# Optimization experiments

Hardware: AMD Instinct MI355X
Metric: run time of the kernel (lower is better)

## Reference

```python
import jax, jax.numpy as jnp
import numpy as np

B, T, E, H = 2, 2048, 1024, 16
D = E // H
K_KEEP = 391
RECENCY = 64
SCALE = D ** -0.5


def setup_inputs() -> dict:
    key = jax.random.key(0)
    k1, k2, k3 = jax.random.split(key, 3)
    x = jax.random.normal(k1, (B, T, E), jnp.float32)
    W_attn = jax.random.normal(k2, (3 * E, E), jnp.float32) * 0.02  # torch Linear weight [out,in]
    W_proj = jax.random.normal(k3, (E, E), jnp.float32) * 0.02
    return {"x": x, "W_attn": W_attn, "W_proj": W_proj}


def reference(x, W_attn, W_proj):
    b, t, c = x.shape
    qkv = x @ W_attn.T                      # [B,T,3E]
    q, k, v = jnp.split(qkv, 3, axis=-1)
    to_heads = lambda u: u.reshape(b, t, H, D).transpose(0, 2, 1, 3)  # [B,H,T,D]
    q, k, v = to_heads(q), to_heads(k), to_heads(v)

    # first pass: causal attention weights for importance scoring
    scores = jnp.einsum('bhqd,bhkd->bhqk', q, k) * SCALE
    causal = jnp.tril(jnp.ones((t, t), dtype=bool))
    scores = jnp.where(causal, scores, -jnp.inf)
    attn_w = jax.nn.softmax(scores, axis=-1)

    # mean importance over query dim, force-keep recent tokens
    imp = attn_w.mean(axis=2)               # [B,H,T]
    imp = imp.at[:, :, -RECENCY:].set(1.0)

    # top-k token selection per (batch, head)
    _, idx = jax.lax.top_k(imp, K_KEEP)     # [B,H,K]

    # gather pruned K/V
    K_keep = jnp.take_along_axis(k, idx[..., None], axis=2)  # [B,H,K,D]
    V_keep = jnp.take_along_axis(v, idx[..., None], axis=2)

    # second attention pass over pruned keys (no causal mask, matches legacy code)
    s2 = jnp.einsum('bhqd,bhkd->bhqk', q, K_keep) * SCALE
    a2 = jax.nn.softmax(s2, axis=-1)
    out = jnp.einsum('bhqk,bhkd->bhqd', a2, V_keep)          # [B,H,T,D]

    out = out.transpose(0, 2, 1, 3).reshape(b, t, c)
    return out @ W_proj.T
```

## Files before the change

kernel.cpp:

```cpp
#include <hip/hip_runtime.h>
#include <hip/hip_bf16.h>


#define TT 2048
#define EE 1024
#define HH 16
#define DD 64
#define KKEEP 391
#define REC 64
#define NBH 32
#define QSCALE 0.125f
#define KPAD 448

typedef short bf16x8 __attribute__((ext_vector_type(8)));
typedef _Float16 f16x8 __attribute__((ext_vector_type(8)));
typedef float f32x4 __attribute__((ext_vector_type(4)));

#define WAIT_VM(N) asm volatile("s_waitcnt vmcnt(" #N ")" ::: "memory")
#define WAIT_LGKM0 asm volatile("s_waitcnt lgkmcnt(0)" ::: "memory")
#define BAR() __builtin_amdgcn_s_barrier()

static __device__ inline unsigned short bf_rn(float x) {
  unsigned u = __float_as_uint(x);
  unsigned r = u + 0x7fffu + ((u >> 16) & 1u);
  return (unsigned short)(r >> 16);
}
static __device__ inline float bf_up(unsigned short h) {
  return __uint_as_float((unsigned)h << 16);
}
static __device__ inline unsigned pkf16(float a, float b) {
  union { _Float16 h[2]; unsigned u; } t;
  t.h[0] = (_Float16)a; t.h[1] = (_Float16)b; return t.u;
}
static __device__ inline void glds16(const void* g, void* l) {
  __builtin_amdgcn_global_load_lds(
      (const __attribute__((address_space(1))) void*)g,
      (__attribute__((address_space(3))) void*)l, 16, 0, 0);
}

static __device__ inline void split4(const float* __restrict__ src,
                                     unsigned short* __restrict__ ho,
                                     unsigned short* __restrict__ lo_, int i)
{
  float4 v = *reinterpret_cast<const float4*>(&src[i]);
  ushort4 hh, ll;
  float f;
  hh.x = bf_rn(v.x); f = bf_up(hh.x); ll.x = bf_rn(v.x - f);
  hh.y = bf_rn(v.y); f = bf_up(hh.y); ll.y = bf_rn(v.y - f);
  hh.z = bf_rn(v.z); f = bf_up(hh.z); ll.z = bf_rn(v.z - f);
  hh.w = bf_rn(v.w); f = bf_up(hh.w); ll.w = bf_rn(v.w - f);
  *reinterpret_cast<ushort4*>(&ho[i]) = hh;
  *reinterpret_cast<ushort4*>(&lo_[i]) = ll;
}

__global__ __launch_bounds__(256) void split_kernel(
    const float* __restrict__ src, unsigned short* __restrict__ ho,
    unsigned short* __restrict__ lo_, int n)
{
  int i = (blockIdx.x * 256 + threadIdx.x) * 4;
  const int stride = gridDim.x * 1024;
  for (; i < n; i += stride) split4(src, ho, lo_, i);
}

__global__ __launch_bounds__(256) void split2_kernel(
    const float* __restrict__ x, const float* __restrict__ wa,
    unsigned short* __restrict__ xh, unsigned short* __restrict__ xl,
    unsigned short* __restrict__ wh, unsigned short* __restrict__ wl)
{
  const int n1 = 4096 * 1024, n2 = 3072 * 1024;
  int i = (blockIdx.x * 256 + threadIdx.x) * 4;
  const int stride = gridDim.x * 1024;
  for (; i < n1 + n2; i += stride) {
    if (i < n1) split4(x, xh, xl, i);
    else        split4(wa, wh, wl, i - n1);
  }
}

template<bool VB, int MODE>
__global__ __launch_bounds__(256) void gemm_pipe(
    const unsigned short* __restrict__ Ah, const unsigned short* __restrict__ Al,
    const unsigned short* __restrict__ Bh, const unsigned short* __restrict__ Bl,
    float* __restrict__ Cc, unsigned short* __restrict__ Qho, unsigned short* __restrict__ Qlo,
    unsigned short* __restrict__ Kho, unsigned short* __restrict__ Klo,
    float* __restrict__ Vo, int M, int N, int Kd, int nOff)
{
  __shared__ __align__(16) unsigned short Ahs[2][128 * 32];
  __shared__ __align__(16) unsigned short Bhs[2][128 * 32];
  __shared__ __align__(16) unsigned short Als[VB ? 1 : 2][128 * 32];
  __shared__ __align__(16) unsigned short Bls[VB ? 1 : 2][128 * 32];
  const int tid = threadIdx.x;
  const int m0 = blockIdx.y * 128, n0 = nOff + blockIdx.x * 128;
  const int w = tid >> 6, lane = tid & 63;
  const int wm = w >> 1, wn = w & 1;
  const int l15 = lane & 15, l4 = lane >> 4;

  size_t gA[2], gB[2]; int ldso[2];
#pragma unroll
  for (int s = 0; s < 2; s++) {
    int seg = w * 2 + s;
    int r = seg * 16 + (lane >> 2);
    int kb = (lane & 3) ^ ((r >> 1) & 3);
    gA[s] = (size_t)(m0 + r) * Kd + kb * 8;
    gB[s] = (size_t)(n0 + r) * Kd + kb * 8;
    ldso[s] = seg * 512;
  }
  auto STAGE = [&](int bb, int k0) {
#pragma unroll
    for (int s = 0; s < 2; s++) {
      glds16(&Ah[gA[s] + k0], &Ahs[bb][ldso[s]]);
      glds16(&Bh[gB[s] + k0], &Bhs[bb][ldso[s]]);
      if (!VB) {
        glds16(&Al[gA[s] + k0], &Als[bb][ldso[s]]);
        glds16(&Bl[gB[s] + k0], &Bls[bb][ldso[s]]);
      }
    }
  };

  f32x4 acc[4][4] = {};

  STAGE(0, 0);
  STAGE(1, 32);
  int cur = 0;
  for (int k0 = 0; k0 < Kd; k0 += 32) {
    if (k0 + 32 < Kd) { if (VB) WAIT_VM(4); else WAIT_VM(8); }
    else WAIT_VM(0);
    BAR();
    bf16x8 ah[4], al[4], bh[4], bl[4];
#pragma unroll
    for (int i = 0; i < 4; i++) {
      int ar = wm * 64 + i * 16 + l15;
      int aoff = ar * 32 + ((l4 ^ ((ar >> 1) & 3)) * 8);
      ah[i] = *reinterpret_cast<const bf16x8*>(&Ahs[cur][aoff]);
      int br = wn * 64 + i * 16 + l15;
      int boff = br * 32 + ((l4 ^ ((br >> 1) & 3)) * 8);
      bh[i] = *reinterpret_cast<const bf16x8*>(&Bhs[cur][boff]);
      if (!VB) {
        al[i] = *reinterpret_cast<const bf16x8*>(&Als[cur][aoff]);
        bl[i] = *reinterpret_cast<const bf16x8*>(&Bls[cur][boff]);
      }
    }
#pragma unroll
    for (int i = 0; i < 4; i++)
#pragma unroll
      for (int j = 0; j < 4; j++) {
        acc[i][j] = __builtin_amdgcn_mfma_f32_16x16x32_bf16(ah[i], bh[j], acc[i][j], 0, 0, 0);
        if (!VB) {
          acc[i][j] = __builtin_amdgcn_mfma_f32_16x16x32_bf16(ah[i], bl[j], acc[i][j], 0, 0, 0);
          acc[i][j] = __builtin_amdgcn_mfma_f32_16x16x32_bf16(al[i], bh[j], acc[i][j], 0, 0, 0);
        }
      }
    WAIT_LGKM0;
    BAR();
    if (k0 + 64 < Kd) STAGE(cur, k0 + 64);
    cur ^= 1;
  }

  if (MODE == 0) {
#pragma unroll
    for (int i = 0; i < 4; i++) {
      int mrow0 = m0 + wm * 64 + i * 16 + l4 * 4;
#pragma unroll
      for (int j = 0; j < 4; j++) {
        int ncol = n0 + wn * 64 + j * 16 + l15;
#pragma unroll
        for (int r = 0; r < 4; r++)
          Cc[(size_t)(mrow0 + r) * N + ncol] = acc[i][j][r];
      }
    }
  } else if (VB) {
#pragma unroll
    for (int j = 0; j < 4; j++) {
      int n = n0 + wn * 64 + j * 16 + l15;
      int rr = n & 1023;
      int h = rr >> 6, d0 = rr & 63;
#pragma unroll
      for (int i = 0; i < 4; i++) {
        int mrow0 = m0 + wm * 64 + i * 16 + l4 * 4;
#pragma unroll
        for (int r = 0; r < 4; r++) {
          int m = mrow0 + r;
          int b = m >> 11, t = m & 2047;
          Vo[((size_t)((b * HH + h) * TT + t)) * DD + d0] = acc[i][j][r];
        }
      }
    }
  } else {
#pragma unroll
    for (int j = 0; j < 4; j++) {
      int n = n0 + wn * 64 + j * 16 + l15;
      int p = n >> 10, rr = n & 1023;
      int h = rr >> 6, d0 = rr & 63;
#pragma unroll
      for (int i = 0; i < 4; i++) {
        int mrow0 = m0 + wm * 64 + i * 16 + l4 * 4;
#pragma unroll
        for (int r = 0; r < 4; r++) {
          int m = mrow0 + r;
          int b = m >> 11, t = m & 2047;
          size_t idx = ((size_t)((b * HH + h) * TT + t)) * DD + d0;
          float v = acc[i][j][r];
          unsigned short hi_ = bf_rn(v);
          unsigned short lo2 = bf_rn(v - bf_up(hi_));
          if (p == 0) { Qho[idx] = hi_; Qlo[idx] = lo2; }
          else        { Kho[idx] = hi_; Klo[idx] = lo2; }
        }
      }
    }
  }
}

__global__ __launch_bounds__(512, 4) void importance6_kernel(
    const unsigned short* __restrict__ Qh, const unsigned short* __restrict__ Ql,
    const unsigned short* __restrict__ Kh, const unsigned short* __restrict__ Kl,
    float* __restrict__ part)
{
  const int bh = blockIdx.x;
  const int rt = blockIdx.z ? (15 - (int)blockIdx.y) : (int)blockIdx.y;
  const int slab = ((int)blockIdx.y << 1) | (int)blockIdx.z;
  const int row0 = rt * 128;
  const int nch = 2 * rt + 2;
  const int tid = threadIdx.x;
  const int w = tid >> 6, lane = tid & 63;
  const int wm = w >> 1, wn = w & 1;
  const int l15 = lane & 15, l4 = lane >> 4;
  __shared__ __align__(16) unsigned short Khs[2][64 * 64];
  __shared__ __align__(16) unsigned short Kls[2][64 * 64];
  __shared__ float csw[8 * 32];
  __shared__ float rsb[2 * 128];

  const int kr = w * 8 + (lane >> 3);
  const int sk8 = (lane & 7) ^ (kr & 7);
  const int ldw = w * 512;
  auto STAGEK1 = [&](int bb, int ci) {
    glds16(&Kh[((size_t)(bh * TT + ci * 64 + kr)) * DD + sk8 * 8], &Khs[bb][ldw]);
  };
  auto STAGEK2 = [&](int bb, int ci) {
    size_t ga = ((size_t)(bh * TT + ci * 64 + kr)) * DD + sk8 * 8;
    glds16(&Kh[ga], &Khs[bb][ldw]);
    glds16(&Kl[ga], &Kls[bb][ldw]);
  };

  bf16x8 aq[2][2];
#pragma unroll
  for (int ks = 0; ks < 2; ks++)
#pragma unroll
    for (int i = 0; i < 2; i++) {
      int ar = wm * 32 + i * 16 + l15;
      size_t ga = ((size_t)(bh * TT + row0 + ar)) * DD + (ks * 4 + l4) * 8;
      aq[ks][i] = *reinterpret_cast<const bf16x8*>(&Qh[ga]);
    }

  float rsum[2][4];
#pragma unroll
  for (int i = 0; i < 2; i++)
#pragma unroll
    for (int r = 0; r < 4; r++) rsum[i][r] = 0.f;

  STAGEK1(0, 0);
  STAGEK1(1, 1);
  int cur = 0;
  for (int ci = 0; ci < nch; ci++) {
    if (ci + 1 < nch) WAIT_VM(1); else WAIT_VM(0);
    BAR();
    f32x4 acc[2][2] = {};
#pragma unroll
    for (int ks = 0; ks < 2; ks++) {
#pragma unroll
      for (int j = 0; j < 2; j++) {
        int br = wn * 32 + j * 16 + l15;
        int off = br * 64 + (((ks * 4 + l4) ^ (br & 7)) * 8);
        bf16x8 bh_ = *reinterpret_cast<const bf16x8*>(&Khs[cur][off]);
#pragma unroll
        for (int i = 0; i < 2; i++)
          acc[i][j] = __builtin_amdgcn_mfma_f32_16x16x32_bf16(aq[ks][i], bh_, acc[i][j], 0, 0, 0);
      }
    }
    if (ci >= 2 * rt) {
#pragma unroll
      for (int i = 0; i < 2; i++)
#pragma unroll
        for (int r = 0; r < 4; r++) {
          int row = row0 + wm * 32 + i * 16 + l4 * 4 + r;
          float s = 0.f;
#pragma unroll
          for (int j = 0; j < 2; j++) {
            int key = ci * 64 + wn * 32 + j * 16 + l15;
            float p = __expf(acc[i][j][r] * QSCALE);
            if (key > row) p = 0.f;
            s += p;
          }
          rsum[i][r] += s;
        }
    } else {
#pragma unroll
      for (int i = 0; i < 2; i++)
#pragma unroll
        for (int r = 0; r < 4; r++) {
          float s = 0.f;
#pragma unroll
          for (int j = 0; j < 2; j++) s += __expf(acc[i][j][r] * QSCALE);
          rsum[i][r] += s;
        }
    }
    WAIT_LGKM0;
    BAR();
    if (ci + 2 < nch) STAGEK1(cur, ci + 2);
    cur ^= 1;
  }
#pragma unroll
  for (int i = 0; i < 2; i++)
#pragma unroll
    for (int r = 0; r < 4; r++) {
      float v = rsum[i][r];
      v += __shfl_xor(v, 1); v += __shfl_xor(v, 2);
      v += __shfl_xor(v, 4); v += __shfl_xor(v, 8);
      rsum[i][r] = v;
    }
  __syncthreads();
  if (l15 == 0) {
#pragma unroll
    for (int i = 0; i < 2; i++)
#pragma unroll
      for (int r = 0; r < 4; r++)
        rsb[wn * 128 + wm * 32 + i * 16 + l4 * 4 + r] = rsum[i][r];
  }
  __syncthreads();
#pragma unroll
  for (int i = 0; i < 2; i++)
#pragma unroll
    for (int r = 0; r < 4; r++) {
      int rl = wm * 32 + i * 16 + l4 * 4 + r;
      rsum[i][r] = 1.0f / (rsb[rl] + rsb[128 + rl]);
    }

  bf16x8 aql[2][2];
#pragma unroll
  for (int ks = 0; ks < 2; ks++)
#pragma unroll
    for (int i = 0; i < 2; i++) {
      int ar = wm * 32 + i * 16 + l15;
      size_t ga = ((size_t)(bh * TT + row0 + ar)) * DD + (ks * 4 + l4) * 8;
      aql[ks][i] = *reinterpret_cast<const bf16x8*>(&Ql[ga]);
    }

  STAGEK2(0, 0);
  STAGEK2(1, 1);
  cur = 0;
  for (int ci = 0; ci < nch; ci++) {
    if (ci + 1 < nch) WAIT_VM(2); else WAIT_VM(0);
    BAR();
    f32x4 acc[2][2] = {};
#pragma unroll
    for (int ks = 0; ks < 2; ks++) {
#pragma unroll
      for (int j = 0; j < 2; j++) {
        int br = wn * 32 + j * 16 + l15;
        int off = br * 64 + (((ks * 4 + l4) ^ (br & 7)) * 8);
        bf16x8 bh_ = *reinterpret_cast<const bf16x8*>(&Khs[cur][off]);
        bf16x8 bl_ = *reinterpret_cast<const bf16x8*>(&Kls[cur][off]);
#pragma unroll
        for (int i = 0; i < 2; i++) {
          acc[i][j] = __builtin_amdgcn_mfma_f32_16x16x32_bf16(aq[ks][i], bh_, acc[i][j], 0, 0, 0);
          acc[i][j] = __builtin_amdgcn_mfma_f32_16x16x32_bf16(aq[ks][i], bl_, acc[i][j], 0, 0, 0);
          acc[i][j] = __builtin_amdgcn_mfma_f32_16x16x32_bf16(aql[ks][i], bh_, acc[i][j], 0, 0, 0);
        }
      }
    }
    float cp[2] = {0.f, 0.f};
    if (ci >= 2 * rt) {
#pragma unroll
      for (int i = 0; i < 2; i++)
#pragma unroll
        for (int r = 0; r < 4; r++) {
          int row = row0 + wm * 32 + i * 16 + l4 * 4 + r;
          float il = rsum[i][r];
#pragma unroll
          for (int j = 0; j < 2; j++) {
            int key = ci * 64 + wn * 32 + j * 16 + l15;
            float p = __expf(acc[i][j][r] * QSCALE) * il;
            if (key > row) p = 0.f;
            cp[j] += p;
          }
        }
    } else {
#pragma unroll
      for (int i = 0; i < 2; i++)
#pragma unroll
        for (int r = 0; r < 4; r++) {
          float il = rsum[i][r];
#pragma unroll
          for (int j = 0; j < 2; j++)
            cp[j] += __expf(acc[i][j][r] * QSCALE) * il;
        }
    }
#pragma unroll
    for (int j = 0; j < 2; j++) {
      float v = cp[j];
      v += __shfl_xor(v, 16); v += __shfl_xor(v, 32);
      cp[j] = v;
    }
    WAIT_LGKM0;
    BAR();
    if (ci + 2 < nch) STAGEK2(cur, ci + 2);
    if (l4 == 0) {
#pragma unroll
      for (int j = 0; j < 2; j++)
        csw[w * 32 + j * 16 + l15] = cp[j];
    }
    WAIT_LGKM0;
    BAR();
    if (tid < 64) {
      int wnc = tid >> 5, cl = tid & 31;
      float s = csw[(0 * 2 + wnc) * 32 + cl] + csw[(1 * 2 + wnc) * 32 + cl] +
                csw[(2 * 2 + wnc) * 32 + cl] + csw[(3 * 2 + wnc) * 32 + cl];
      part[((size_t)(bh * 16 + slab)) * 2048 + ci * 64 + tid] = s;
    }
    cur ^= 1;
  }
}

__global__ __launch_bounds__(256) void topk_gather_kernel(
    const float* __restrict__ part,
    const unsigned short* __restrict__ Kh, const unsigned short* __restrict__ Kl,
    const float* __restrict__ V,
    unsigned short* __restrict__ Kf, unsigned short* __restrict__ Vt)
{
  const int bh = blockIdx.x, tid = threadIdx.x;
  const int lane = tid & 63, w = tid >> 6;
  __shared__ int redi[4];
  __shared__ int stot;
  __shared__ int base[256];
  __shared__ int idxb[KKEEP];
  unsigned u[8];
#pragma unroll
  for (int k = 0; k < 8; k++) {
    int e = tid * 8 + k;
    float s = 0.f;
#pragma unroll
    for (int p = 0; p < 16; p++) {
      int rtp = (p & 1) ? 15 - (p >> 1) : (p >> 1);
      if (e < (rtp + 1) * 128) s += part[((size_t)(bh * 16 + p)) * 2048 + e];
    }
    float v = (e >= TT - REC) ? 3.0e3f : s;
    u[k] = __float_as_uint(v);
  }
  unsigned lo = 0u, hi = 0x7f800000u;
  for (int it = 0; it < 31; it++) {
    unsigned mid = lo + ((hi - lo + 1) >> 1);
    int c = 0;
#pragma unroll
    for (int k = 0; k < 8; k++) c += (u[k] >= mid) ? 1 : 0;
#pragma unroll
    for (int off = 1; off <= 32; off <<= 1) c += __shfl_xor(c, off);
    if (lane == 0) redi[w] = c;
    __syncthreads();
    int tot = redi[0] + redi[1] + redi[2] + redi[3];
    if (tot >= KKEEP) lo = mid; else hi = mid - 1;
    __syncthreads();
  }
  const unsigned vstar = lo;
  int cgt = 0, ceq = 0;
#pragma unroll
  for (int k = 0; k < 8; k++) { cgt += (u[k] > vstar) ? 1 : 0; ceq += (u[k] == vstar) ? 1 : 0; }
  base[tid] = cgt; __syncthreads();
  if (tid == 0) {
    int run = 0;
    for (int i = 0; i < 256; i++) { int t = base[i]; base[i] = run; run += t; }
    stot = run;
  }
  __syncthreads();
  int off1 = base[tid];
#pragma unroll
  for (int k = 0; k < 8; k++)
    if (u[k] > vstar) idxb[off1++] = tid * 8 + k;
  __syncthreads();
  base[tid] = ceq; __syncthreads();
  if (tid == 0) {
    int run = 0;
    for (int i = 0; i < 256; i++) { int t = base[i]; base[i] = run; run += t; }
  }
  __syncthreads();
  int off2 = stot + base[tid];
#pragma unroll
  for (int k = 0; k < 8; k++)
    if (u[k] == vstar) { if (off2 < KKEEP) idxb[off2] = tid * 8 + k; off2++; }
  __syncthreads();
  for (int f = tid; f < KPAD * 8; f += 256) {
    int kk = f >> 3, c8 = f & 7;
    union { _Float16 h[8]; uint4 v; } o;
#pragma unroll
    for (int j = 0; j < 8; j++) o.h[j] = (_Float16)0.f;
    if (kk < KKEEP) {
      int sr = idxb[kk];
      bf16x8 hv = *reinterpret_cast<const bf16x8*>(&Kh[((size_t)(bh * TT + sr)) * DD + c8 * 8]);
      bf16x8 lv = *reinterpret_cast<const bf16x8*>(&Kl[((size_t)(bh * TT + sr)) * DD + c8 * 8]);
#pragma unroll
      for (int j = 0; j < 8; j++)
        o.h[j] = (_Float16)(bf_up((unsigned short)hv[j]) + bf_up((unsigned short)lv[j]));
    }
    *reinterpret_cast<uint4*>(&Kf[((size_t)(bh * KPAD) + kk) * DD + c8 * 8]) = o.v;
  }
  for (int f = tid; f < KPAD * 8; f += 256) {
    int kk = f >> 3, d8 = f & 7;
    float vv[8];
#pragma unroll
    for (int j = 0; j < 8; j++) vv[j] = 0.f;
    if (kk < KKEEP) {
      int sr = idxb[kk];
      float4 a = *reinterpret_cast<const float4*>(&V[((size_t)(bh * TT + sr)) * DD + d8 * 8]);
      float4 b = *reinterpret_cast<const float4*>(&V[((size_t)(bh * TT + sr)) * DD + d8 * 8 + 4]);
      vv[0] = a.x; vv[1] = a.y; vv[2] = a.z; vv[3] = a.w;
      vv[4] = b.x; vv[5] = b.y; vv[6] = b.z; vv[7] = b.w;
    }
#pragma unroll
    for (int j = 0; j < 8; j++) {
      union { _Float16 h; unsigned short s; } t;
      t.h = (_Float16)vv[j];
      Vt[((size_t)(bh * DD) + d8 * 8 + j) * KPAD + kk] = t.s;
    }
  }
}

__global__ __launch_bounds__(256) void attn4_kernel(
    const unsigned short* __restrict__ Qh, const unsigned short* __restrict__ Ql,
    const unsigned short* __restrict__ Kf, const unsigned short* __restrict__ Vt,
    unsigned short* __restrict__ AOh, unsigned short* __restrict__ AOl)
{
  const int rt = blockIdx.y, bh = blockIdx.x;
  const int tid = threadIdx.x;
  const int w = tid >> 6, lane = tid & 63;
  const int l15 = lane & 15, l4 = lane >> 4;
  __shared__ __align__(16) unsigned short Qs[64 * 64];
  __shared__ __align__(16) unsigned short Ks[2][64 * 64];
  __shared__ __align__(16) unsigned short Vs[2][64 * 64];
  __shared__ float LDSo[4][64][16];
  const int row0 = rt * 64;

  int srow[2], skb[2], slds[2];
#pragma unroll
  for (int s = 0; s < 2; s++) {
    int seg = w * 2 + s;
    int r = seg * 8 + (lane >> 3);
    int k8 = lane & 7;
    srow[s] = r; skb[s] = k8 ^ (r & 7); slds[s] = seg * 512;
  }
  auto STAGEA = [&](int bb, int ci) {
#pragma unroll
    for (int s = 0; s < 2; s++) {
      glds16(&Kf[((size_t)(bh * KPAD) + ci * 64 + srow[s]) * DD + skb[s] * 8], &Ks[bb][slds[s]]);
      glds16(&Vt[((size_t)(bh * DD) + srow[s]) * KPAD + ci * 64 + skb[s] * 8], &Vs[bb][slds[s]]);
    }
  };

#pragma unroll
  for (int it = 0; it < 2; it++) {
    int idx = it * 256 + tid;
    int r = idx >> 3, k8 = idx & 7;
    size_t ga = ((size_t)(bh * TT + row0 + r)) * DD + k8 * 8;
    bf16x8 hv = *reinterpret_cast<const bf16x8*>(&Qh[ga]);
    bf16x8 lv = *reinterpret_cast<const bf16x8*>(&Ql[ga]);
    union { _Float16 h[8]; uint4 v; } q16;
#pragma unroll
    for (int j = 0; j < 8; j++)
      q16.h[j] = (_Float16)(bf_up((unsigned short)hv[j]) + bf_up((unsigned short)lv[j]));
    *reinterpret_cast<uint4*>(&Qs[r * 64 + ((k8 ^ (r & 7)) * 8)]) = q16.v;
  }
  STAGEA(0, 0);
  STAGEA(1, 1);
  WAIT_LGKM0;
  BAR();
  f16x8 bq[2];
#pragma unroll
  for (int ks = 0; ks < 2; ks++) {
    int br = w * 16 + l15;
    bq[ks] = *reinterpret_cast<const f16x8*>(&Qs[br * 64 + (((ks * 4 + l4) ^ (br & 7)) * 8)]);
  }

  f32x4 acc_o[4] = {};
  float rsum = 0.f;
  int cur = 0;

  for (int ci = 0; ci < 7; ci++) {
    if (ci + 1 < 7) WAIT_VM(4); else WAIT_VM(0);
    BAR();
    f32x4 accs[4] = {};
#pragma unroll
    for (int ks = 0; ks < 2; ks++) {
#pragma unroll
      for (int i = 0; i < 4; i++) {
        int kr = i * 16 + l15;
        f16x8 af = *reinterpret_cast<const f16x8*>(&Ks[cur][kr * 64 + (((ks * 4 + l4) ^ (kr & 7)) * 8)]);
        accs[i] = __builtin_amdgcn_mfma_f32_16x16x32_f16(af, bq[ks], accs[i], 0, 0, 0);
      }
    }
    float p[4][4];
#pragma unroll
    for (int i = 0; i < 4; i++)
#pragma unroll
      for (int r = 0; r < 4; r++) {
        int gk = ci * 64 + i * 16 + l4 * 4 + r;
        float pp = __expf(accs[i][r] * QSCALE);
        if (gk >= KKEEP) pp = 0.f;
        p[i][r] = pp;
        rsum += pp;
      }
    unsigned pkU[4][2];
#pragma unroll
    for (int i = 0; i < 4; i++) {
      pkU[i][0] = pkf16(p[i][0], p[i][1]);
      pkU[i][1] = pkf16(p[i][2], p[i][3]);
    }
#pragma unroll
    for (int ks = 0; ks < 2; ks++) {
      union { f16x8 h; unsigned u[4]; } bp;
#pragma unroll
      for (int wp = 0; wp < 4; wp++) {
        int src = ((l4 & 1) * 2 + (wp >> 1)) * 16 + l15;
        unsigned v0 = (unsigned)__shfl((int)pkU[ks * 2][wp & 1], src);
        unsigned v1 = (unsigned)__shfl((int)pkU[ks * 2 + 1][wp & 1], src);
        bp.u[wp] = (l4 & 2) ? v1 : v0;
      }
#pragma unroll
      for (int i = 0; i < 4; i++) {
        int dr = i * 16 + l15;
        f16x8 av = *reinterpret_cast<const f16x8*>(&Vs[cur][dr * 64 + (((ks * 4 + l4) ^ (dr & 7)) * 8)]);
        acc_o[i] = __builtin_amdgcn_mfma_f32_16x16x32_f16(av, bp.h, acc_o[i], 0, 0, 0);
      }
    }
    WAIT_LGKM0;
    BAR();
    if (ci + 2 < 7) STAGEA(cur, ci + 2);
    cur ^= 1;
  }
  rsum += __shfl_xor(rsum, 16);
  rsum += __shfl_xor(rsum, 32);
  float inv = 1.0f / rsum;
#pragma unroll
  for (int i = 0; i < 4; i++)
#pragma unroll
    for (int r = 0; r < 4; r++)
      LDSo[w][i * 16 + l4 * 4 + r][l15] = acc_o[i][r] * inv;
  __syncthreads();
  const int b = bh >> 4, h = bh & 15;
#pragma unroll
  for (int uu = 0; uu < 2; uu++) {
    int u = uu * 64 + lane;
    int q = u >> 3, dc = u & 7;
    int row = row0 + w * 16 + q;
    union { unsigned short s[8]; uint4 v; } sh, sl;
#pragma unroll
    for (int j = 0; j < 8; j++) {
      float v = LDSo[w][dc * 8 + j][q];
      unsigned short hh = bf_rn(v);
      sh.s[j] = hh;
      sl.s[j] = bf_rn(v - bf_up(hh));
    }
    size_t addr = ((size_t)(b * TT + row)) * EE + h * DD + dc * 8;
    *reinterpret_cast<uint4*>(&AOh[addr]) = sh.v;
    *reinterpret_cast<uint4*>(&AOl[addr]) = sl.v;
  }
}

extern "C" void kernel_launch(void* const* d_in, const int* in_sizes, int n_in,
                              void* d_out, int out_size, void* d_ws, size_t ws_size,
                              hipStream_t stream)
{
  const float* x     = (const float*)d_in[0];
  const float* Wattn = (const float*)d_in[1];
  const float* Wproj = (const float*)d_in[2];
  float* out = (float*)d_out;
  float* ws  = (float*)d_ws;

  const size_t SZQ = (size_t)NBH * TT * DD;
  const size_t SZK = (size_t)NBH * KPAD * DD;
  float* Vb   = ws;
  float* part = Vb + SZQ;
  unsigned short* Kf  = (unsigned short*)(part + (size_t)NBH * 16 * TT);
  unsigned short* Vt  = Kf + SZK;
  unsigned short* Qhp = Vt + SZK;
  unsigned short* Qlp = Qhp + SZQ;
  unsigned short* Khp = Qlp + SZQ;
  unsigned short* Klp = Khp + SZQ;
  unsigned short* xh  = Klp + SZQ;
  unsigned short* xl  = xh + (size_t)4096 * 1024;
  unsigned short* Wh  = xl + (size_t)4096 * 1024;
  unsigned short* Wl  = Wh + (size_t)3072 * 1024;
  unsigned short* AOh = xh;
  unsigned short* AOl = xl;
  unsigned short* Ph  = Wh;
  unsigned short* Pl  = Ph + (size_t)1024 * 1024;

  const size_t needB =
      ((size_t)SZQ + (size_t)NBH * 16 * TT) * 4 +
      ((size_t)2 * SZK + (size_t)4 * SZQ + (size_t)2 * 4096 * 1024 + (size_t)2 * 3072 * 1024) * 2;
  if (ws_size < needB) return;

  split2_kernel<<<1024, 256, 0, stream>>>(x, Wattn, xh, xl, Wh, Wl);
  gemm_pipe<false, 1><<<dim3(16, 32), 256, 0, stream>>>(xh, xl, Wh, Wl, nullptr,
      Qhp, Qlp, Khp, Klp, nullptr, 4096, 3072, 1024, 0);
  gemm_pipe<true, 1><<<dim3(8, 32), 256, 0, stream>>>(xh, xl, Wh, Wl, nullptr,
      nullptr, nullptr, nullptr, nullptr, Vb, 4096, 3072, 1024, 2048);
  split_kernel<<<256, 256, 0, stream>>>(Wproj, Ph, Pl, 1024 * 1024);
  importance6_kernel<<<dim3(NBH, 8, 2), 512, 0, stream>>>(Qhp, Qlp, Khp, Klp, part);
  topk_gather_kernel<<<NBH, 256, 0, stream>>>(part, Khp, Klp, Vb, Kf, Vt);
  attn4_kernel<<<dim3(NBH, 32), 256, 0, stream>>>(Qhp, Qlp, Kf, Vt, AOh, AOl);
  gemm_pipe<false, 0><<<dim3(8, 32), 256, 0, stream>>>(AOh, AOl, Ph, Pl, out,
      nullptr, nullptr, nullptr, nullptr, nullptr, 4096, 1024, 1024, 0);
}
```

Measured before the change: 269.2 us.

## Split-K the output projection GEMM and reorder importance blocks heaviest-first

The output projection GEMM now runs as a two-way split-K over a 3D grid, doubling the block count from 256 to 512 to fill more CUs. Each half writes fp32 partials into the dead Q buffers, and a new add kernel sums them into the output. The importance kernel grid is flattened to 16 slabs with the heaviest row tiles launched first, and the top-k reducer's slab-to-tile mapping is updated to match. The cost is an extra kernel launch plus extra fp32 write and read traffic for the partials.

```diff
diff --git a/kernel.cpp b/kernel.cpp
--- a/kernel.cpp
+++ b/kernel.cpp
@@ -76,13 +76,27 @@
   }
 }
 
+__global__ __launch_bounds__(256) void add_kernel(
+    const float* __restrict__ p0, const float* __restrict__ p1,
+    float* __restrict__ out, int n)
+{
+  int i = (blockIdx.x * 256 + threadIdx.x) * 4;
+  const int stride = gridDim.x * 1024;
+  for (; i < n; i += stride) {
+    float4 a = *reinterpret_cast<const float4*>(&p0[i]);
+    float4 b = *reinterpret_cast<const float4*>(&p1[i]);
+    *reinterpret_cast<float4*>(&out[i]) =
+        make_float4(a.x + b.x, a.y + b.y, a.z + b.z, a.w + b.w);
+  }
+}
+
 template<bool VB, int MODE>
 __global__ __launch_bounds__(256) void gemm_pipe(
     const unsigned short* __restrict__ Ah, const unsigned short* __restrict__ Al,
     const unsigned short* __restrict__ Bh, const unsigned short* __restrict__ Bl,
     float* __restrict__ Cc, unsigned short* __restrict__ Qho, unsigned short* __restrict__ Qlo,
     unsigned short* __restrict__ Kho, unsigned short* __restrict__ Klo,
-    float* __restrict__ Vo, int M, int N, int Kd, int nOff)
+    float* __restrict__ Vo, int M, int N, int Kd, int ldAB, int nOff)
 {
   __shared__ __align__(16) unsigned short Ahs[2][128 * 32];
   __shared__ __align__(16) unsigned short Bhs[2][128 * 32];
@@ -90,6 +104,7 @@
   __shared__ __align__(16) unsigned short Bls[VB ? 1 : 2][128 * 32];
   const int tid = threadIdx.x;
   const int m0 = blockIdx.y * 128, n0 = nOff + blockIdx.x * 128;
+  const int kOff = blockIdx.z * Kd;
   const int w = tid >> 6, lane = tid & 63;
   const int wm = w >> 1, wn = w & 1;
   const int l15 = lane & 15, l4 = lane >> 4;
@@ -100,8 +115,8 @@
     int seg = w * 2 + s;
     int r = seg * 16 + (lane >> 2);
     int kb = (lane & 3) ^ ((r >> 1) & 3);
-    gA[s] = (size_t)(m0 + r) * Kd + kb * 8;
-    gB[s] = (size_t)(n0 + r) * Kd + kb * 8;
+    gA[s] = (size_t)(m0 + r) * ldAB + kOff + kb * 8;
+    gB[s] = (size_t)(n0 + r) * ldAB + kOff + kb * 8;
     ldso[s] = seg * 512;
   }
   auto STAGE = [&](int bb, int k0) {
@@ -156,6 +171,7 @@
   }
 
   if (MODE == 0) {
+    float* Cout = Cc + (size_t)blockIdx.z * ((size_t)M * N);
 #pragma unroll
     for (int i = 0; i < 4; i++) {
       int mrow0 = m0 + wm * 64 + i * 16 + l4 * 4;
@@ -164,7 +180,7 @@
         int ncol = n0 + wn * 64 + j * 16 + l15;
 #pragma unroll
         for (int r = 0; r < 4; r++)
-          Cc[(size_t)(mrow0 + r) * N + ncol] = acc[i][j][r];
+          Cout[(size_t)(mrow0 + r) * N + ncol] = acc[i][j][r];
       }
     }
   } else if (VB) {
@@ -215,8 +231,9 @@
     float* __restrict__ part)
 {
   const int bh = blockIdx.x;
-  const int rt = blockIdx.z ? (15 - (int)blockIdx.y) : (int)blockIdx.y;
-  const int slab = ((int)blockIdx.y << 1) | (int)blockIdx.z;
+  const int y = (int)blockIdx.y;
+  const int rt = (y < 8) ? (15 - y) : (y - 8);
+  const int slab = y;
   const int row0 = rt * 128;
   const int nch = 2 * rt + 2;
   const int tid = threadIdx.x;
@@ -438,7 +455,7 @@
     float s = 0.f;
 #pragma unroll
     for (int p = 0; p < 16; p++) {
-      int rtp = (p & 1) ? 15 - (p >> 1) : (p >> 1);
+      int rtp = (p < 8) ? (15 - p) : (p - 8);
       if (e < (rtp + 1) * 128) s += part[((size_t)(bh * 16 + p)) * 2048 + e];
     }
     float v = (e >= TT - REC) ? 3.0e3f : s;
@@ -689,6 +706,8 @@
   unsigned short* AOl = xl;
   unsigned short* Ph  = Wh;
   unsigned short* Pl  = Ph + (size_t)1024 * 1024;
+  float* pb0 = (float*)Qhp;
+  float* pb1 = pb0 + SZQ;
 
   const size_t needB =
       ((size_t)SZQ + (size_t)NBH * 16 * TT) * 4 +
@@ -697,13 +716,14 @@
 
   split2_kernel<<<1024, 256, 0, stream>>>(x, Wattn, xh, xl, Wh, Wl);
   gemm_pipe<false, 1><<<dim3(16, 32), 256, 0, stream>>>(xh, xl, Wh, Wl, nullptr,
-      Qhp, Qlp, Khp, Klp, nullptr, 4096, 3072, 1024, 0);
+      Qhp, Qlp, Khp, Klp, nullptr, 4096, 3072, 1024, 1024, 0);
   gemm_pipe<true, 1><<<dim3(8, 32), 256, 0, stream>>>(xh, xl, Wh, Wl, nullptr,
-      nullptr, nullptr, nullptr, nullptr, Vb, 4096, 3072, 1024, 2048);
+      nullptr, nullptr, nullptr, nullptr, Vb, 4096, 3072, 1024, 1024, 2048);
   split_kernel<<<256, 256, 0, stream>>>(Wproj, Ph, Pl, 1024 * 1024);
-  importance6_kernel<<<dim3(NBH, 8, 2), 512, 0, stream>>>(Qhp, Qlp, Khp, Klp, part);
+  importance6_kernel<<<dim3(NBH, 16), 512, 0, stream>>>(Qhp, Qlp, Khp, Klp, part);
   topk_gather_kernel<<<NBH, 256, 0, stream>>>(part, Khp, Klp, Vb, Kf, Vt);
   attn4_kernel<<<dim3(NBH, 32), 256, 0, stream>>>(Qhp, Qlp, Kf, Vt, AOh, AOl);
-  gemm_pipe<false, 0><<<dim3(8, 32), 256, 0, stream>>>(AOh, AOl, Ph, Pl, out,
-      nullptr, nullptr, nullptr, nullptr, nullptr, 4096, 1024, 1024, 0);
-}
+  gemm_pipe<false, 0><<<dim3(8, 32, 2), 256, 0, stream>>>(AOh, AOl, Ph, Pl, pb0,
+      nullptr, nullptr, nullptr, nullptr, nullptr, 4096, 1024, 512, 1024, 0);
+  add_kernel<<<2048, 256, 0, stream>>>(pb0, pb1, out, 4096 * 1024);
+}
```

After: 265.2 us. About the same (-1.5%).
